# Optimization experiments

Measured on AMD Instinct MI355X. Metric: run time of the kernel, lower is better.

Reference implementation:

```python
import jax, jax.numpy as jnp
import numpy as np

DIM = 2048


def setup_inputs() -> dict:
    key = jax.random.key(0)
    ks = jax.random.split(key, 9)
    scale = 1.0 / np.sqrt(DIM)
    x = jax.random.normal(ks[0], (4, 4096, DIM), dtype=jnp.float32)
    def lin(kw, kb):
        W = jax.random.uniform(kw, (DIM, DIM), jnp.float32, -scale, scale)
        b = jax.random.uniform(kb, (DIM,), jnp.float32, -scale, scale)
        return W, b
    Wq, bq = lin(ks[1], ks[2])
    Wk, bk = lin(ks[3], ks[4])
    Wv, bv = lin(ks[5], ks[6])
    Wg, bg = lin(ks[7], ks[8])
    return {"x": x, "Wq": Wq, "bq": bq, "Wk": Wk, "bk": bk,
            "Wv": Wv, "bv": bv, "Wg": Wg, "bg": bg}


def reference(x, Wq, bq, Wk, bk, Wv, bv, Wg, bg):
    # torch nn.Linear: y = x @ W.T + b
    q = jnp.einsum('bsd,ed->bse', x, Wq) + bq
    k = jnp.einsum('bsd,ed->bse', x, Wk) + bk
    v = jnp.einsum('bsd,ed->bse', x, Wv) + bv
    g = jax.nn.sigmoid(jnp.einsum('bsd,ed->bse', x, Wg) + bg)
    kv_state = jnp.cumsum(k * v, axis=1)  # O(N) associative state along seq
    return q * kv_state * g
```

## Files before the change

kernel.cpp:

```cpp
#include <hip/hip_runtime.h>
#include <stdint.h>

#define DIM   2048
#define BATCH 4
#define SEQ   4096
#define NTOK  (BATCH*SEQ)
#define NCH   256
#define CHUNK (SEQ/NCH)

#define XB_BYTES   ((size_t)NTOK*DIM*2)
#define WB_BYTES   ((size_t)4*DIM*DIM*2)
#define PW_BYTES   ((size_t)2*NTOK*DIM*2)
#define PART_BYTES ((size_t)BATCH*NCH*DIM*4)

typedef __bf16 bf16x8 __attribute__((ext_vector_type(8)));
typedef float  f32x4  __attribute__((ext_vector_type(4)));

__device__ __forceinline__ unsigned short f2bf(float f) {
  unsigned int u = __float_as_uint(f);
  u += 0x7FFFu + ((u >> 16) & 1u);
  return (unsigned short)(u >> 16);
}
__device__ __forceinline__ float bflo(unsigned int u){ return __uint_as_float(u << 16); }
__device__ __forceinline__ float bfhi(unsigned int u){ return __uint_as_float(u & 0xFFFF0000u); }
__device__ __forceinline__ float sigm(float x){ return 1.0f/(1.0f + __expf(-x)); }

__device__ __forceinline__ void gload16(const void* g, void* l) {
  __builtin_amdgcn_global_load_lds((const __attribute__((address_space(1))) unsigned int*)g,
                                   (__attribute__((address_space(3))) unsigned int*)l,
                                   16, 0, 0);
}

__global__ void cvt_kernel(const float* __restrict__ src,
                           unsigned short* __restrict__ dst, int n8) {
  int i = blockIdx.x * blockDim.x + threadIdx.x;
  if (i >= n8) return;
  const float4* s4 = (const float4*)src;
  float4 a = s4[2*i], b = s4[2*i+1];
  uint4 o;
  o.x = (unsigned int)f2bf(a.x) | ((unsigned int)f2bf(a.y) << 16);
  o.y = (unsigned int)f2bf(a.z) | ((unsigned int)f2bf(a.w) << 16);
  o.z = (unsigned int)f2bf(b.x) | ((unsigned int)f2bf(b.y) << 16);
  o.w = (unsigned int)f2bf(b.z) | ((unsigned int)f2bf(b.w) << 16);
  ((uint4*)dst)[i] = o;
}

__global__ void cvt_w_kernel(const float* __restrict__ Wq, const float* __restrict__ Wk,
                             const float* __restrict__ Wv, const float* __restrict__ Wg,
                             unsigned short* __restrict__ dst) {
  const int z = blockIdx.y;
  const float* src = (z == 0) ? Wq : (z == 1) ? Wk : (z == 2) ? Wv : Wg;
  int i = blockIdx.x * blockDim.x + threadIdx.x;
  const float4* s4 = (const float4*)src;
  float4 a = s4[2*i], b = s4[2*i+1];
  uint4 o;
  o.x = (unsigned int)f2bf(a.x) | ((unsigned int)f2bf(a.y) << 16);
  o.y = (unsigned int)f2bf(a.z) | ((unsigned int)f2bf(a.w) << 16);
  o.z = (unsigned int)f2bf(b.x) | ((unsigned int)f2bf(b.y) << 16);
  o.w = (unsigned int)f2bf(b.z) | ((unsigned int)f2bf(b.w) << 16);
  ((uint4*)(dst + (size_t)z * DIM * DIM))[i] = o;
}

__global__ __launch_bounds__(256, 2)
void gemm_kernel(const unsigned short* __restrict__ xb,
                 const unsigned short* __restrict__ Wall,
                 const float* __restrict__ bq, const float* __restrict__ bk,
                 const float* __restrict__ bv, const float* __restrict__ bg,
                 unsigned short* __restrict__ Yw,
                 unsigned short* __restrict__ Yp) {
  __shared__ __align__(16) unsigned short ldsA [128*32];
  __shared__ __align__(16) unsigned short ldsBa[128*32];
  __shared__ __align__(16) unsigned short ldsBb[128*32];

  const int t  = threadIdx.x;
  const int e0 = blockIdx.x * 128;
  const int m0 = blockIdx.y * 128;
  const int zg = blockIdx.z;
  const unsigned short* Wa = Wall + (size_t)(zg == 0 ? 0 : 1) * DIM * DIM;
  const unsigned short* Wb = Wall + (size_t)(zg == 0 ? 3 : 2) * DIM * DIM;

  const int r0 = t >> 2;
  const int cc = (t & 3) ^ (r0 & 3);
  const unsigned short* gA0 = xb + (size_t)(m0 + r0) * DIM + cc * 8;
  const unsigned short* gA1 = gA0 + (size_t)64 * DIM;
  const unsigned short* gBa0 = Wa + (size_t)(e0 + r0) * DIM + cc * 8;
  const unsigned short* gBa1 = gBa0 + (size_t)64 * DIM;
  const unsigned short* gBb0 = Wb + (size_t)(e0 + r0) * DIM + cc * 8;
  const unsigned short* gBb1 = gBb0 + (size_t)64 * DIM;
  unsigned short* lA0  = &ldsA [(size_t)t * 8];
  unsigned short* lA1  = &ldsA [(size_t)(t + 256) * 8];
  unsigned short* lBa0 = &ldsBa[(size_t)t * 8];
  unsigned short* lBa1 = &ldsBa[(size_t)(t + 256) * 8];
  unsigned short* lBb0 = &ldsBb[(size_t)t * 8];
  unsigned short* lBb1 = &ldsBb[(size_t)(t + 256) * 8];

  const int lane = t & 63;
  const int wave = t >> 6;
  const int wm = wave >> 1, wn = wave & 1;
  const int lr = lane & 15, lq = lane >> 4;
  const int swz8 = (lq ^ (lr & 3)) * 8;
  int aoff[4], boff[4];
  #pragma unroll
  for (int i = 0; i < 4; i++) aoff[i] = (wm*64 + i*16 + lr)*32 + swz8;
  #pragma unroll
  for (int j = 0; j < 4; j++) boff[j] = (wn*64 + j*16 + lr)*32 + swz8;

  f32x4 accA[4][4], accB[4][4];
  #pragma unroll
  for (int i = 0; i < 4; i++)
    #pragma unroll
    for (int j = 0; j < 4; j++) {
      accA[i][j] = (f32x4){0.f, 0.f, 0.f, 0.f};
      accB[i][j] = (f32x4){0.f, 0.f, 0.f, 0.f};
    }

  for (int kt = 0; kt < DIM/32; ++kt) {
    __syncthreads();
    const int ko = kt * 32;
    gload16(gA0  + ko, lA0);
    gload16(gA1  + ko, lA1);
    gload16(gBa0 + ko, lBa0);
    gload16(gBa1 + ko, lBa1);
    gload16(gBb0 + ko, lBb0);
    gload16(gBb1 + ko, lBb1);
    __syncthreads();

    bf16x8 a[4];
    #pragma unroll
    for (int i = 0; i < 4; i++) a[i] = *(const bf16x8*)&ldsA[aoff[i]];
    {
      bf16x8 b[4];
      #pragma unroll
      for (int j = 0; j < 4; j++) b[j] = *(const bf16x8*)&ldsBa[boff[j]];
      #pragma unroll
      for (int i = 0; i < 4; i++)
        #pragma unroll
        for (int j = 0; j < 4; j++)
          accA[i][j] = __builtin_amdgcn_mfma_f32_16x16x32_bf16(a[i], b[j], accA[i][j], 0, 0, 0);
    }
    {
      bf16x8 b[4];
      #pragma unroll
      for (int j = 0; j < 4; j++) b[j] = *(const bf16x8*)&ldsBb[boff[j]];
      #pragma unroll
      for (int i = 0; i < 4; i++)
        #pragma unroll
        for (int j = 0; j < 4; j++)
          accB[i][j] = __builtin_amdgcn_mfma_f32_16x16x32_bf16(a[i], b[j], accB[i][j], 0, 0, 0);
    }
  }

  const float* biasA = (zg == 0) ? bq : bk;
  const float* biasB = (zg == 0) ? bg : bv;
  unsigned short* Y = (zg == 0) ? Yw : Yp;
  #pragma unroll
  for (int j = 0; j < 4; j++) {
    const int e = e0 + wn*64 + j*16 + lr;
    const float bA = biasA[e];
    const float bB = biasB[e];
    #pragma unroll
    for (int i = 0; i < 4; i++) {
      const int mb = m0 + wm*64 + i*16 + lq*4;
      #pragma unroll
      for (int r = 0; r < 4; r++) {
        const float vA = accA[i][j][r] + bA;
        const float vB = accB[i][j][r] + bB;
        const float val = (zg == 0) ? (vA * sigm(vB)) : (vA * vB);
        Y[(size_t)(mb + r) * DIM + e] = f2bf(val);
      }
    }
  }
}

__global__ void chunk_sum_kernel(const unsigned short* __restrict__ Yp,
                                 float* __restrict__ partial) {
  const int d8 = threadIdx.x;
  const int c = blockIdx.y, b = blockIdx.z;
  const size_t base = (size_t)(b*SEQ + c*CHUNK) * (DIM/8) + d8;
  const uint4* pp = (const uint4*)Yp + base;
  float s[8] = {0.f,0.f,0.f,0.f,0.f,0.f,0.f,0.f};
  #pragma unroll 4
  for (int i = 0; i < CHUNK; i++) {
    uint4 pu = pp[(size_t)i*(DIM/8)];
    s[0] += bflo(pu.x);  s[1] += bfhi(pu.x);
    s[2] += bflo(pu.y);  s[3] += bfhi(pu.y);
    s[4] += bflo(pu.z);  s[5] += bfhi(pu.z);
    s[6] += bflo(pu.w);  s[7] += bfhi(pu.w);
  }
  float4* po = (float4*)(partial + (size_t)(b*NCH + c)*DIM + d8*8);
  po[0] = make_float4(s[0], s[1], s[2], s[3]);
  po[1] = make_float4(s[4], s[5], s[6], s[7]);
}

__global__ void scan_kernel(float* __restrict__ partial) {
  const int wid  = (blockIdx.x * blockDim.x + threadIdx.x) >> 6;
  const int lane = threadIdx.x & 63;
  const int b = wid >> 11;
  const int d = wid & (DIM - 1);
  float* base = partial + (size_t)b * NCH * DIM + d;
  float v[4];
  #pragma unroll
  for (int k = 0; k < 4; k++) v[k] = base[(size_t)(lane*4 + k) * DIM];
  float sum = v[0] + v[1] + v[2] + v[3];
  float inc = sum;
  #pragma unroll
  for (int off = 1; off < 64; off <<= 1) {
    float n = __shfl_up(inc, off, 64);
    if (lane >= off) inc += n;
  }
  float run = inc - sum;
  #pragma unroll
  for (int k = 0; k < 4; k++) {
    base[(size_t)(lane*4 + k) * DIM] = run;
    run += v[k];
  }
}

__global__ void final_kernel(const unsigned short* __restrict__ Yw,
                             const unsigned short* __restrict__ Yp,
                             const float* __restrict__ partial,
                             float* __restrict__ out) {
  const int d8 = threadIdx.x;
  const int c = blockIdx.y, b = blockIdx.z;
  const size_t base = (size_t)(b*SEQ + c*CHUNK) * (DIM/8) + d8;
  const float4* pst = (const float4*)(partial + (size_t)(b*NCH + c)*DIM + d8*8);
  float4 st0 = pst[0], st1 = pst[1];
  float s[8] = {st0.x, st0.y, st0.z, st0.w, st1.x, st1.y, st1.z, st1.w};
  const uint4* pw = (const uint4*)Yw + base;
  const uint4* pp = (const uint4*)Yp + base;
  float4* po = (float4*)out + base*2;
  #pragma unroll 2
  for (int i = 0; i < CHUNK; i++) {
    uint4 pu = pp[(size_t)i*(DIM/8)];
    uint4 wu = pw[(size_t)i*(DIM/8)];
    s[0] += bflo(pu.x);  s[1] += bfhi(pu.x);
    s[2] += bflo(pu.y);  s[3] += bfhi(pu.y);
    s[4] += bflo(pu.z);  s[5] += bfhi(pu.z);
    s[6] += bflo(pu.w);  s[7] += bfhi(pu.w);
    float4 o0, o1;
    o0.x = bflo(wu.x)*s[0];  o0.y = bfhi(wu.x)*s[1];
    o0.z = bflo(wu.y)*s[2];  o0.w = bfhi(wu.y)*s[3];
    o1.x = bflo(wu.z)*s[4];  o1.y = bfhi(wu.z)*s[5];
    o1.z = bflo(wu.w)*s[6];  o1.w = bfhi(wu.w)*s[7];
    po[(size_t)i*(DIM/4)]     = o0;
    po[(size_t)i*(DIM/4) + 1] = o1;
  }
}

extern "C" void kernel_launch(void* const* d_in, const int* in_sizes, int n_in,
                              void* d_out, int out_size, void* d_ws, size_t ws_size,
                              hipStream_t stream) {
  const float* x  = (const float*)d_in[0];
  const float* Wq = (const float*)d_in[1];
  const float* bq = (const float*)d_in[2];
  const float* Wk = (const float*)d_in[3];
  const float* bk = (const float*)d_in[4];
  const float* Wv = (const float*)d_in[5];
  const float* bv = (const float*)d_in[6];
  const float* Wg = (const float*)d_in[7];
  const float* bg = (const float*)d_in[8];
  float* out = (float*)d_out;

  char* ws = (char*)d_ws;
  unsigned short* xb      = (unsigned short*)(ws);
  unsigned short* Wall    = (unsigned short*)(ws + XB_BYTES);
  unsigned short* Yw      = (unsigned short*)(ws + XB_BYTES + WB_BYTES);
  unsigned short* Yp      = Yw + (size_t)NTOK * DIM;
  float*          partial = (float*)(ws + XB_BYTES + WB_BYTES + PW_BYTES);

  {
    int n8 = NTOK * DIM / 8;
    cvt_kernel<<<n8 / 256, 256, 0, stream>>>(x, xb, n8);
    int w8 = DIM * DIM / 8;
    cvt_w_kernel<<<dim3(w8 / 256, 4), 256, 0, stream>>>(Wq, Wk, Wv, Wg, Wall);
  }

  gemm_kernel<<<dim3(DIM/128, NTOK/128, 2), 256, 0, stream>>>(
      xb, Wall, bq, bk, bv, bg, Yw, Yp);

  chunk_sum_kernel<<<dim3(1, NCH, BATCH), 256, 0, stream>>>(Yp, partial);
  scan_kernel<<<(BATCH*DIM*64)/256, 256, 0, stream>>>(partial);
  final_kernel<<<dim3(1, NCH, BATCH), 256, 0, stream>>>(Yw, Yp, partial, out);
}
```

Baseline: 901.5 us.

## Rewrite fused GEMM with 256x128 tiles, BK=64 double-buffered LDS pipeline

Reworks the dual-projection GEMM to 512 threads and 256-row M tiles that share the weight tiles. K tiles grow to 64, and a two-buffer LDS ping-pong issues global-to-LDS loads for upcoming tiles between MFMA phases, using explicit vmcnt/lgkmcnt waits, raw barriers and s_setprio. The goal is to hide global load latency and raise the arithmetic intensity of the loads. In exchange it uses 128KB of LDS per block, which may limit occupancy, and it depends on fragile hand-tuned wait counts.

```diff
diff --git a/kernel.cpp b/kernel.cpp
--- a/kernel.cpp
+++ b/kernel.cpp
@@ -61,50 +61,82 @@
   ((uint4*)(dst + (size_t)z * DIM * DIM))[i] = o;
 }
 
-__global__ __launch_bounds__(256, 2)
+#define BK    64
+#define NKT   (DIM/BK)
+#define NIT   (NKT/2)
+
+#define A0_OFF 0
+#define A1_OFF 8192
+#define BA_OFF 16384
+#define BB_OFF 24576
+
+#define STG(Lb, HOFF, GP, TILE) do {                        \
+    const unsigned short* _g = (GP) + (TILE) * BK;          \
+    unsigned short* _l = (Lb) + (HOFF) + t * 8;             \
+    gload16(_g, _l);                                        \
+    gload16(_g + (size_t)64 * DIM, _l + 4096);              \
+  } while (0)
+
+#define LDA(L) do { _Pragma("unroll")                       \
+    for (int i = 0; i < 4; i++) {                           \
+      afr[i][0] = *(const bf16x8*)&(L)[arow[i] + sw0];      \
+      afr[i][1] = *(const bf16x8*)&(L)[arow[i] + sw1]; } } while (0)
+
+#define LDB(L, BOFF, J0) do { _Pragma("unroll")                        \
+    for (int j = 0; j < 2; j++) {                                      \
+      bfr[j][0] = *(const bf16x8*)&(L)[(BOFF) + brow[(J0)+j] + sw0];   \
+      bfr[j][1] = *(const bf16x8*)&(L)[(BOFF) + brow[(J0)+j] + sw1]; } } while (0)
+
+#define MM16(ACC, J0) do { _Pragma("unroll")                                     \
+    for (int kk = 0; kk < 2; kk++) { _Pragma("unroll")                           \
+      for (int i = 0; i < 4; i++) { _Pragma("unroll")                            \
+        for (int j = 0; j < 2; j++) {                                            \
+          ACC[i][(J0)+j] = __builtin_amdgcn_mfma_f32_16x16x32_bf16(              \
+              afr[i][kk], bfr[j][kk], ACC[i][(J0)+j], 0, 0, 0); } } } } while (0)
+
+#define BARR()  __builtin_amdgcn_s_barrier()
+#define LGKM0() asm volatile("s_waitcnt lgkmcnt(0)" ::: "memory")
+#define VMC6()  asm volatile("s_waitcnt vmcnt(6)" ::: "memory")
+#define VMC0()  asm volatile("s_waitcnt vmcnt(0)" ::: "memory")
+
+__global__ __launch_bounds__(512, 2)
 void gemm_kernel(const unsigned short* __restrict__ xb,
                  const unsigned short* __restrict__ Wall,
                  const float* __restrict__ bq, const float* __restrict__ bk,
                  const float* __restrict__ bv, const float* __restrict__ bg,
                  unsigned short* __restrict__ Yw,
                  unsigned short* __restrict__ Yp) {
-  __shared__ __align__(16) unsigned short ldsA [128*32];
-  __shared__ __align__(16) unsigned short ldsBa[128*32];
-  __shared__ __align__(16) unsigned short ldsBb[128*32];
+  __shared__ __align__(16) unsigned short lds[2][32768];
 
   const int t  = threadIdx.x;
   const int e0 = blockIdx.x * 128;
-  const int m0 = blockIdx.y * 128;
+  const int m0 = blockIdx.y * 256;
   const int zg = blockIdx.z;
   const unsigned short* Wa = Wall + (size_t)(zg == 0 ? 0 : 1) * DIM * DIM;
   const unsigned short* Wb = Wall + (size_t)(zg == 0 ? 3 : 2) * DIM * DIM;
 
-  const int r0 = t >> 2;
-  const int cc = (t & 3) ^ (r0 & 3);
-  const unsigned short* gA0 = xb + (size_t)(m0 + r0) * DIM + cc * 8;
-  const unsigned short* gA1 = gA0 + (size_t)64 * DIM;
-  const unsigned short* gBa0 = Wa + (size_t)(e0 + r0) * DIM + cc * 8;
-  const unsigned short* gBa1 = gBa0 + (size_t)64 * DIM;
-  const unsigned short* gBb0 = Wb + (size_t)(e0 + r0) * DIM + cc * 8;
-  const unsigned short* gBb1 = gBb0 + (size_t)64 * DIM;
-  unsigned short* lA0  = &ldsA [(size_t)t * 8];
-  unsigned short* lA1  = &ldsA [(size_t)(t + 256) * 8];
-  unsigned short* lBa0 = &ldsBa[(size_t)t * 8];
-  unsigned short* lBa1 = &ldsBa[(size_t)(t + 256) * 8];
-  unsigned short* lBb0 = &ldsBb[(size_t)t * 8];
-  unsigned short* lBb1 = &ldsBb[(size_t)(t + 256) * 8];
-
-  const int lane = t & 63;
-  const int wave = t >> 6;
+  const int srow = t >> 3;
+  const int csrc = (t & 7) ^ (srow & 7);
+  const unsigned short* gA0 = xb + (size_t)(m0 + srow) * DIM + csrc * 8;
+  const unsigned short* gA1 = gA0 + (size_t)128 * DIM;
+  const unsigned short* gBa = Wa + (size_t)(e0 + srow) * DIM + csrc * 8;
+  const unsigned short* gBb = Wb + (size_t)(e0 + srow) * DIM + csrc * 8;
+
+  unsigned short* L0 = &lds[0][0];
+  unsigned short* L1 = &lds[1][0];
+
+  const int lane = t & 63, wave = t >> 6;
   const int wm = wave >> 1, wn = wave & 1;
   const int lr = lane & 15, lq = lane >> 4;
-  const int swz8 = (lq ^ (lr & 3)) * 8;
-  int aoff[4], boff[4];
-  #pragma unroll
-  for (int i = 0; i < 4; i++) aoff[i] = (wm*64 + i*16 + lr)*32 + swz8;
-  #pragma unroll
-  for (int j = 0; j < 4; j++) boff[j] = (wn*64 + j*16 + lr)*32 + swz8;
-
+  const int sw0 = ((0 + lq) ^ (lr & 7)) * 8;
+  const int sw1 = ((4 + lq) ^ (lr & 7)) * 8;
+  int arow[4], brow[4];
+  #pragma unroll
+  for (int i = 0; i < 4; i++) arow[i] = (wm * 64 + i * 16 + lr) * 64;
+  #pragma unroll
+  for (int j = 0; j < 4; j++) brow[j] = (wn * 64 + j * 16 + lr) * 64;
+
+  bf16x8 afr[4][2], bfr[2][2];
   f32x4 accA[4][4], accB[4][4];
   #pragma unroll
   for (int i = 0; i < 4; i++)
@@ -114,40 +146,60 @@
       accB[i][j] = (f32x4){0.f, 0.f, 0.f, 0.f};
     }
 
-  for (int kt = 0; kt < DIM/32; ++kt) {
-    __syncthreads();
-    const int ko = kt * 32;
-    gload16(gA0  + ko, lA0);
-    gload16(gA1  + ko, lA1);
-    gload16(gBa0 + ko, lBa0);
-    gload16(gBa1 + ko, lBa1);
-    gload16(gBb0 + ko, lBb0);
-    gload16(gBb1 + ko, lBb1);
-    __syncthreads();
-
-    bf16x8 a[4];
-    #pragma unroll
-    for (int i = 0; i < 4; i++) a[i] = *(const bf16x8*)&ldsA[aoff[i]];
-    {
-      bf16x8 b[4];
-      #pragma unroll
-      for (int j = 0; j < 4; j++) b[j] = *(const bf16x8*)&ldsBa[boff[j]];
-      #pragma unroll
-      for (int i = 0; i < 4; i++)
-        #pragma unroll
-        for (int j = 0; j < 4; j++)
-          accA[i][j] = __builtin_amdgcn_mfma_f32_16x16x32_bf16(a[i], b[j], accA[i][j], 0, 0, 0);
-    }
-    {
-      bf16x8 b[4];
-      #pragma unroll
-      for (int j = 0; j < 4; j++) b[j] = *(const bf16x8*)&ldsBb[boff[j]];
-      #pragma unroll
-      for (int i = 0; i < 4; i++)
-        #pragma unroll
-        for (int j = 0; j < 4; j++)
-          accB[i][j] = __builtin_amdgcn_mfma_f32_16x16x32_bf16(a[i], b[j], accB[i][j], 0, 0, 0);
-    }
+  STG(L0, A0_OFF, gA0, 0);
+  STG(L0, A1_OFF, gA1, 0);
+  STG(L0, BA_OFF, gBa, 0);
+  STG(L0, BB_OFF, gBb, 0);
+  STG(L1, A0_OFF, gA0, 1);
+  STG(L1, A1_OFF, gA1, 1);
+  STG(L1, BA_OFF, gBa, 1);
+  VMC6();
+  BARR();
+
+  #pragma unroll 1
+  for (int it = 0; it < NIT; ++it) {
+    const int T1 = 2 * it + 1, T2 = 2 * it + 2, T3 = 2 * it + 3;
+    const bool nl = (it != NIT - 1);
+    LDA(L0); LDB(L0, BA_OFF, 0);
+    STG(L1, BB_OFF, gBb, T1);
+    BARR(); LGKM0();
+    __builtin_amdgcn_s_setprio(1); MM16(accA, 0); __builtin_amdgcn_s_setprio(0);
+    BARR();
+    LDB(L0, BB_OFF, 0);
+    if (nl) STG(L0, A0_OFF, gA0, T2);
+    BARR(); LGKM0();
+    __builtin_amdgcn_s_setprio(1); MM16(accB, 0); __builtin_amdgcn_s_setprio(0);
+    BARR();
+    LDB(L0, BA_OFF, 2);
+    if (nl) STG(L0, A1_OFF, gA1, T2);
+    BARR(); LGKM0();
+    __builtin_amdgcn_s_setprio(1); MM16(accA, 2); __builtin_amdgcn_s_setprio(0);
+    BARR();
+    LDB(L0, BB_OFF, 2);
+    if (nl) { STG(L0, BA_OFF, gBa, T2); VMC6(); } else { VMC0(); }
+    BARR(); LGKM0();
+    __builtin_amdgcn_s_setprio(1); MM16(accB, 2); __builtin_amdgcn_s_setprio(0);
+    BARR();
+    LDA(L1); LDB(L1, BA_OFF, 0);
+    if (nl) STG(L0, BB_OFF, gBb, T2);
+    BARR(); LGKM0();
+    __builtin_amdgcn_s_setprio(1); MM16(accA, 0); __builtin_amdgcn_s_setprio(0);
+    BARR();
+    LDB(L1, BB_OFF, 0);
+    if (nl) STG(L1, A0_OFF, gA0, T3);
+    BARR(); LGKM0();
+    __builtin_amdgcn_s_setprio(1); MM16(accB, 0); __builtin_amdgcn_s_setprio(0);
+    BARR();
+    LDB(L1, BA_OFF, 2);
+    if (nl) STG(L1, A1_OFF, gA1, T3);
+    BARR(); LGKM0();
+    __builtin_amdgcn_s_setprio(1); MM16(accA, 2); __builtin_amdgcn_s_setprio(0);
+    BARR();
+    LDB(L1, BB_OFF, 2);
+    if (nl) { STG(L1, BA_OFF, gBa, T3); VMC6(); }
+    BARR(); LGKM0();
+    __builtin_amdgcn_s_setprio(1); MM16(accB, 2); __builtin_amdgcn_s_setprio(0);
+    BARR();
   }
 
   const float* biasA = (zg == 0) ? bq : bk;
@@ -155,12 +207,12 @@
   unsigned short* Y = (zg == 0) ? Yw : Yp;
   #pragma unroll
   for (int j = 0; j < 4; j++) {
-    const int e = e0 + wn*64 + j*16 + lr;
+    const int e = e0 + wn * 64 + j * 16 + lr;
     const float bA = biasA[e];
     const float bB = biasB[e];
     #pragma unroll
     for (int i = 0; i < 4; i++) {
-      const int mb = m0 + wm*64 + i*16 + lq*4;
+      const int mb = m0 + wm * 64 + i * 16 + lq * 4;
       #pragma unroll
       for (int r = 0; r < 4; r++) {
         const float vA = accA[i][j][r] + bA;
@@ -275,7 +327,7 @@
     cvt_w_kernel<<<dim3(w8 / 256, 4), 256, 0, stream>>>(Wq, Wk, Wv, Wg, Wall);
   }
 
-  gemm_kernel<<<dim3(DIM/128, NTOK/128, 2), 256, 0, stream>>>(
+  gemm_kernel<<<dim3(DIM/128, NTOK/256, 2), 512, 0, stream>>>(
       xb, Wall, bq, bk, bv, bg, Yw, Yp);
 
   chunk_sum_kernel<<<dim3(1, NCH, BATCH), 256, 0, stream>>>(Yp, partial);
```

Result: faster. 819.2 us (-9.1%).
